# Performance work log

Measured on AMD Instinct MI355X. Metric: run time of the kernel, lower is better.

## Reference

```python
import jax, jax.numpy as jnp
import numpy as np

NUM_HEADS = 32
NUM_KV_HEADS = 8
HEAD_DIM = 128
ROPE_BASE = 10000.0
EPS = 1e-6


def rotate_half(x):
    x1, x2 = jnp.split(x, 2, axis=-1)
    return jnp.concatenate((-x2, x1), axis=-1)


def rms_norm(x, w):
    var = jnp.mean(x * x, axis=-1, keepdims=True)
    return w * (x * jax.lax.rsqrt(var + EPS))


def setup_inputs() -> dict:
    key = jax.random.key(0)
    ks = jax.random.split(key, 5)
    B, S, H = 2, 2048, 4096
    hidden_states = jax.random.normal(ks[0], (B, S, H), dtype=jnp.float32)
    position_ids = jnp.broadcast_to(jnp.arange(S, dtype=jnp.int64), (B, S))
    sc = 1.0 / np.sqrt(H)
    Wq = jax.random.normal(ks[1], (NUM_HEADS * HEAD_DIM, H), dtype=jnp.float32) * sc
    Wk = jax.random.normal(ks[2], (NUM_KV_HEADS * HEAD_DIM, H), dtype=jnp.float32) * sc
    Wv = jax.random.normal(ks[3], (NUM_KV_HEADS * HEAD_DIM, H), dtype=jnp.float32) * sc
    Wo = jax.random.normal(ks[4], (H, NUM_HEADS * HEAD_DIM), dtype=jnp.float32) * sc
    q_norm_w = jnp.ones((HEAD_DIM,), dtype=jnp.float32)
    k_norm_w = jnp.ones((HEAD_DIM,), dtype=jnp.float32)
    return {"hidden_states": hidden_states, "position_ids": position_ids,
            "Wq": Wq, "Wk": Wk, "Wv": Wv, "Wo": Wo,
            "q_norm_w": q_norm_w, "k_norm_w": k_norm_w}


def reference(hidden_states, position_ids, Wq, Wk, Wv, Wo, q_norm_w, k_norm_w):
    B, S, H = hidden_states.shape
    nh, nkv, hd = NUM_HEADS, NUM_KV_HEADS, HEAD_DIM
    groups = nh // nkv

    # QKV projections (Linear, no bias: y = x @ W.T)
    q = (hidden_states @ Wq.T).reshape(B, S, nh, hd)
    k = (hidden_states @ Wk.T).reshape(B, S, nkv, hd)
    v = (hidden_states @ Wv.T).reshape(B, S, nkv, hd)

    # QK RMSNorm over head_dim
    q = rms_norm(q, q_norm_w)
    k = rms_norm(k, k_norm_w)

    # RoPE: cos/sin per position, shape [B, S, hd]
    inv_freq = 1.0 / (ROPE_BASE ** (jnp.arange(0, hd, 2, dtype=jnp.float32) / hd))
    freqs = position_ids.astype(jnp.float32)[..., None] * inv_freq  # [B,S,hd/2]
    emb = jnp.concatenate((freqs, freqs), axis=-1)
    cos = jnp.cos(emb)[:, :, None, :]  # [B,S,1,hd]
    sin = jnp.sin(emb)[:, :, None, :]
    q = q * cos + rotate_half(q) * sin
    k = k * cos + rotate_half(k) * sin

    # GQA: repeat KV heads (repeat_interleave along head axis)
    k = jnp.repeat(k, groups, axis=2)  # [B,S,nh,hd]
    v = jnp.repeat(v, groups, axis=2)

    # Causal SDPA
    scale = 1.0 / np.sqrt(hd)
    scores = jnp.einsum('bqhd,bkhd->bhqk', q, k) * scale
    causal = jnp.tril(jnp.ones((S, S), dtype=bool))
    scores = jnp.where(causal, scores, jnp.finfo(scores.dtype).min)
    probs = jax.nn.softmax(scores, axis=-1)
    attn = jnp.einsum('bhqk,bkhd->bqhd', probs, v).reshape(B, S, nh * hd)

    return attn @ Wo.T
```

## Files before the change

kernel.cpp:

```cpp
#include <hip/hip_runtime.h>

typedef __bf16 bf16;
typedef __bf16 bf16x8 __attribute__((ext_vector_type(8)));
typedef __bf16 bf16x4 __attribute__((ext_vector_type(4)));
typedef float  f32x4  __attribute__((ext_vector_type(4)));

__device__ __forceinline__ void async_copy16(const bf16* g, bf16* l) {
    __builtin_amdgcn_global_load_lds(
        (const __attribute__((address_space(1))) unsigned int*)g,
        (__attribute__((address_space(3))) unsigned int*)l, 16, 0, 0);
}

__global__ __launch_bounds__(256) void cast_bf16(const float* __restrict__ src,
                                                 bf16* __restrict__ dst,
                                                 long long n) {
    long long i = ((long long)blockIdx.x * 256 + threadIdx.x) * 8;
    if (i >= n) return;
    float4 v0 = *(const float4*)&src[i];
    float4 v1 = *(const float4*)&src[i + 4];
    union { int4 v; bf16 h[8]; } u;
    u.h[0] = (bf16)v0.x; u.h[1] = (bf16)v0.y; u.h[2] = (bf16)v0.z; u.h[3] = (bf16)v0.w;
    u.h[4] = (bf16)v1.x; u.h[5] = (bf16)v1.y; u.h[6] = (bf16)v1.z; u.h[7] = (bf16)v1.w;
    *(int4*)&dst[i] = u.v;
}

template <typename OutT>
__global__ __launch_bounds__(256) void gemm_bt(const bf16* __restrict__ A,
                                               const bf16* __restrict__ B,
                                               OutT* __restrict__ C,
                                               int M, int N, int K) {
    __shared__ __attribute__((aligned(16))) bf16 lA[128 * 32];
    __shared__ __attribute__((aligned(16))) bf16 lB[128 * 32];
    const int tid = threadIdx.x, lane = tid & 63, w = tid >> 6;
    const int l16 = lane & 15, quad = lane >> 4;
    const int m0 = blockIdx.y * 128, n0 = blockIdx.x * 128;
    const int wm = (w >> 1) * 64, wn = (w & 1) * 64;

    const int sr = lane >> 2;
    const int sc = (lane & 3) * 8;

    f32x4 acc[4][4];
    for (int mi = 0; mi < 4; ++mi)
        for (int ni = 0; ni < 4; ++ni)
            acc[mi][ni] = f32x4{0.f, 0.f, 0.f, 0.f};

    for (int kb = 0; kb < K; kb += 32) {
        for (int i = 0; i < 2; ++i) {
            int c = i * 4 + w;
            async_copy16(&A[(size_t)(m0 + c * 16 + sr) * K + kb + sc],
                         &lA[c * 512 + lane * 8]);
        }
        for (int i = 0; i < 2; ++i) {
            int c = i * 4 + w;
            async_copy16(&B[(size_t)(n0 + c * 16 + sr) * K + kb + sc],
                         &lB[c * 512 + lane * 8]);
        }
        __syncthreads();
        bf16x8 af[4], bfr[4];
        for (int mi = 0; mi < 4; ++mi)
            af[mi] = *(const bf16x8*)&lA[(wm + mi * 16 + l16) * 32 + quad * 8];
        for (int ni = 0; ni < 4; ++ni)
            bfr[ni] = *(const bf16x8*)&lB[(wn + ni * 16 + l16) * 32 + quad * 8];
        for (int mi = 0; mi < 4; ++mi)
            for (int ni = 0; ni < 4; ++ni)
                acc[mi][ni] = __builtin_amdgcn_mfma_f32_16x16x32_bf16(
                    af[mi], bfr[ni], acc[mi][ni], 0, 0, 0);
        __syncthreads();
    }
    for (int mi = 0; mi < 4; ++mi)
        for (int ni = 0; ni < 4; ++ni) {
            int col = n0 + wn + ni * 16 + l16;
            for (int r = 0; r < 4; ++r) {
                int row = m0 + wm + mi * 16 + quad * 4 + r;
                C[(size_t)row * N + col] = (OutT)acc[mi][ni][r];
            }
        }
}

__global__ __launch_bounds__(256) void rmsnorm_rope(const bf16* __restrict__ qkv,
                                                    const float* __restrict__ qw,
                                                    const float* __restrict__ kw,
                                                    bf16* __restrict__ qb,
                                                    bf16* __restrict__ kb) {
    const int lane = threadIdx.x & 63, w = threadIdx.x >> 6;
    const int j = blockIdx.y * 4 + w;
    const int t = blockIdx.x;
    const int b = t >> 11, s = t & 2047;
    const bool isq = (j < 32);
    const bf16* src = qkv + (size_t)t * 6144 + (isq ? j * 128 : 4096 + (j - 32) * 128);
    float a  = (float)src[lane];
    float bb = (float)src[lane + 64];
    float ss = a * a + bb * bb;
    for (int off = 1; off < 64; off <<= 1) ss += __shfl_xor(ss, off, 64);
    float rms = rsqrtf(ss * (1.f / 128.f) + 1e-6f);
    const float* wn = isq ? qw : kw;
    float an = a * rms * wn[lane];
    float bn = bb * rms * wn[lane + 64];
    float inv_freq = exp2f(-(float)lane * (13.287712379549449f / 64.f));
    float fr = (float)s * inv_freq;
    float c = cosf(fr), sn = sinf(fr);
    float o0 = an * c - bn * sn;
    float o1 = bn * c + an * sn;
    if (isq) {
        const float sc = 0.08838834764831845f * 1.4426950408889634f;
        o0 *= sc; o1 *= sc;
    }
    bf16* dst = isq ? (qb + (((size_t)(b * 32 + j)) * 2048 + s) * 128)
                    : (kb + (((size_t)(b * 8 + (j - 32))) * 2048 + s) * 128);
    dst[lane]      = (bf16)o0;
    dst[lane + 64] = (bf16)o1;
}

__global__ __launch_bounds__(256) void v_transpose(const bf16* __restrict__ qkv,
                                                   bf16* __restrict__ vb) {
    __shared__ __attribute__((aligned(16))) bf16 tile[64][130];
    const int tid = threadIdx.x;
    const int tt = blockIdx.x, kvh = blockIdx.y, b = blockIdx.z;
    const bf16* src = qkv + ((size_t)(b * 2048 + tt * 64)) * 6144 + 5120 + kvh * 128;
    for (int i = 0; i < 4; ++i) {
        int idx = tid + i * 256;
        int r = idx >> 4, c8 = (idx & 15) * 8;
        union { int4 v; bf16 h[8]; } u;
        u.v = *(const int4*)&src[(size_t)r * 6144 + c8];
        for (int jj = 0; jj < 8; ++jj) tile[r][c8 + jj] = u.h[jj];
    }
    __syncthreads();
    bf16* dst = vb + ((size_t)(b * 8 + kvh) * 128) * 2048 + tt * 64;
    for (int i = 0; i < 4; ++i) {
        int idx = tid + i * 256;
        int d = idx >> 3, r8 = (idx & 7) * 8;
        union { int4 v; bf16 h[8]; } u;
        for (int jj = 0; jj < 8; ++jj) u.h[jj] = tile[r8 + jj][d];
        *(int4*)&dst[(size_t)d * 2048 + r8] = u.v;
    }
}

__global__ __launch_bounds__(256, 2) void flash_kernel(const bf16* __restrict__ qb,
                                                       const bf16* __restrict__ kb,
                                                       const bf16* __restrict__ vb,
                                                       bf16* __restrict__ attnb) {
    const int S = 2048;
    const int hp = blockIdx.x;
    const int qt = 31 - blockIdx.y;
    const int b  = blockIdx.z;
    const int h0 = hp * 2, kvh = h0 >> 2;
    const int tid = threadIdx.x, lane = tid & 63, w = tid >> 6;
    const int l16 = lane & 15, quad = lane >> 4;

    __shared__ __attribute__((aligned(16))) bf16 lK[64 * 128];
    __shared__ __attribute__((aligned(16))) bf16 lVt[128 * 64];

    const bf16* Qg0 = qb + (((size_t)(b * 32 + h0)) * S + qt * 64 + w * 16 + l16) * 128;
    const bf16* Qg1 = Qg0 + (size_t)S * 128;
    bf16x8 qf0[4], qf1[4];
    for (int c = 0; c < 4; ++c) {
        qf0[c] = *(const bf16x8*)&Qg0[c * 32 + quad * 8];
        qf1[c] = *(const bf16x8*)&Qg1[c * 32 + quad * 8];
    }

    const bf16* Kg = kb + ((size_t)(b * 8 + kvh)) * S * 128;
    const bf16* Vg = vb + ((size_t)(b * 8 + kvh)) * 128 * S;

    int kOff[4], vOff[4];
    bf16 *kDst[4], *vDst[4];
    for (int i = 0; i < 4; ++i) {
        int c = w * 4 + i;
        int rho = c * 4 + (lane >> 4);
        int prow = (rho & 32) | ((rho & 12) << 1) | ((rho & 16) >> 2) | (rho & 3);
        kOff[i] = prow * 128 + (lane & 15) * 8;
        kDst[i] = lK + c * 512 + lane * 8;
        int d = c * 8 + (lane >> 3);
        vOff[i] = d * S + (lane & 7) * 8;
        vDst[i] = lVt + c * 512 + lane * 8;
    }

    float m0_i = -INFINITY, l0_i = 0.f, m1_i = -INFINITY, l1_i = 0.f;
    f32x4 O0[8], O1[8];
    for (int ti = 0; ti < 8; ++ti) { O0[ti] = f32x4{0.f,0.f,0.f,0.f}; O1[ti] = f32x4{0.f,0.f,0.f,0.f}; }

    for (int kt = 0; kt <= qt; ++kt) {
        const bf16* Kt = Kg + (size_t)kt * 64 * 128;
        const bf16* Vt = Vg + kt * 64;
        for (int i = 0; i < 4; ++i) async_copy16(Kt + kOff[i], kDst[i]);
        for (int i = 0; i < 4; ++i) async_copy16(Vt + vOff[i], vDst[i]);
        __syncthreads();

        f32x4 sT0[4], sT1[4];
        for (int mi = 0; mi < 4; ++mi) { sT0[mi] = f32x4{0.f,0.f,0.f,0.f}; sT1[mi] = f32x4{0.f,0.f,0.f,0.f}; }
        for (int mi = 0; mi < 4; ++mi)
            for (int c = 0; c < 4; ++c) {
                bf16x8 kf = *(const bf16x8*)&lK[(mi * 16 + l16) * 128 + c * 32 + quad * 8];
                sT0[mi] = __builtin_amdgcn_mfma_f32_16x16x32_bf16(kf, qf0[c], sT0[mi], 0, 0, 0);
                sT1[mi] = __builtin_amdgcn_mfma_f32_16x16x32_bf16(kf, qf1[c], sT1[mi], 0, 0, 0);
            }

        if (kt == qt) {
            int qloc = w * 16 + l16;
            for (int mi = 0; mi < 4; ++mi) {
                int kvbase = (mi >> 1) * 32 + quad * 8 + (mi & 1) * 4;
                for (int r = 0; r < 4; ++r)
                    if (kvbase + r > qloc) { sT0[mi][r] = -INFINITY; sT1[mi][r] = -INFINITY; }
            }
        }

        float mx0 = sT0[0][0], mx1 = sT1[0][0];
        for (int mi = 0; mi < 4; ++mi)
            for (int r = 0; r < 4; ++r) { mx0 = fmaxf(mx0, sT0[mi][r]); mx1 = fmaxf(mx1, sT1[mi][r]); }
        mx0 = fmaxf(mx0, __shfl_xor(mx0, 16, 64));
        mx0 = fmaxf(mx0, __shfl_xor(mx0, 32, 64));
        mx1 = fmaxf(mx1, __shfl_xor(mx1, 16, 64));
        mx1 = fmaxf(mx1, __shfl_xor(mx1, 32, 64));
        float mn0 = fmaxf(m0_i, mx0), mn1 = fmaxf(m1_i, mx1);
        float al0 = exp2f(m0_i - mn0), al1 = exp2f(m1_i - mn1);
        m0_i = mn0; m1_i = mn1;

        bf16x8 pbt0[2], pbt1[2];
        float s0 = 0.f, s1 = 0.f;
        for (int mi = 0; mi < 4; ++mi) {
            int t = mi >> 1, o = (mi & 1) * 4;
            for (int r = 0; r < 4; ++r) {
                float p0 = exp2f(sT0[mi][r] - mn0);
                float p1 = exp2f(sT1[mi][r] - mn1);
                s0 += p0; s1 += p1;
                pbt0[t][o + r] = (bf16)p0;
                pbt1[t][o + r] = (bf16)p1;
            }
        }
        s0 += __shfl_xor(s0, 16, 64); s0 += __shfl_xor(s0, 32, 64);
        s1 += __shfl_xor(s1, 16, 64); s1 += __shfl_xor(s1, 32, 64);
        l0_i = l0_i * al0 + s0;
        l1_i = l1_i * al1 + s1;
        for (int ti = 0; ti < 8; ++ti) { O0[ti] *= al0; O1[ti] *= al1; }

        for (int ti = 0; ti < 8; ++ti)
            for (int t = 0; t < 2; ++t) {
                bf16x8 vf = *(const bf16x8*)&lVt[(ti * 16 + l16) * 64 + t * 32 + quad * 8];
                O0[ti] = __builtin_amdgcn_mfma_f32_16x16x32_bf16(vf, pbt0[t], O0[ti], 0, 0, 0);
                O1[ti] = __builtin_amdgcn_mfma_f32_16x16x32_bf16(vf, pbt1[t], O1[ti], 0, 0, 0);
            }
        __syncthreads();
    }

    float i0 = 1.f / l0_i, i1 = 1.f / l1_i;
    bf16* dst = attnb + (((size_t)(b * S + qt * 64 + w * 16 + l16)) * 4096) + h0 * 128 + quad * 4;
    for (int ti = 0; ti < 8; ++ti) {
        bf16x4 o4, o5;
        for (int r = 0; r < 4; ++r) { o4[r] = (bf16)(O0[ti][r] * i0); o5[r] = (bf16)(O1[ti][r] * i1); }
        *(bf16x4*)&dst[ti * 16] = o4;
        *(bf16x4*)&dst[128 + ti * 16] = o5;
    }
}

extern "C" void kernel_launch(void* const* d_in, const int* in_sizes, int n_in,
                              void* d_out, int out_size, void* d_ws, size_t ws_size,
                              hipStream_t stream) {
    const float* X  = (const float*)d_in[0];
    const float* Wq = (const float*)d_in[2];
    const float* Wk = (const float*)d_in[3];
    const float* Wv = (const float*)d_in[4];
    const float* Wo = (const float*)d_in[5];
    const float* qw = (const float*)d_in[6];
    const float* kw = (const float*)d_in[7];
    float* out = (float*)d_out;
    char* ws = (char*)d_ws;

    bf16* Xb    = (bf16*)(ws);
    bf16* Wqkvb = (bf16*)(ws + 33554432);
    bf16* QKVb  = (bf16*)(ws + 83886080);
    bf16* qbuf  = (bf16*)(ws);
    bf16* kbuf  = (bf16*)(ws + 33554432);
    bf16* vbuf  = (bf16*)(ws + 41943040);
    bf16* Wob   = (bf16*)(ws + 50331648);
    bf16* attnb = (bf16*)(ws + 83886080);

    cast_bf16<<<8192, 256, 0, stream>>>(X, Xb, 16777216);
    cast_bf16<<<8192, 256, 0, stream>>>(Wq, Wqkvb, 16777216);
    cast_bf16<<<2048, 256, 0, stream>>>(Wk, Wqkvb + 16777216, 4194304);
    cast_bf16<<<2048, 256, 0, stream>>>(Wv, Wqkvb + 20971520, 4194304);

    gemm_bt<bf16><<<dim3(48, 32), 256, 0, stream>>>(Xb, Wqkvb, QKVb, 4096, 6144, 4096);

    rmsnorm_rope<<<dim3(4096, 10), 256, 0, stream>>>(QKVb, qw, kw, qbuf, kbuf);
    v_transpose<<<dim3(32, 8, 2), 256, 0, stream>>>(QKVb, vbuf);
    cast_bf16<<<8192, 256, 0, stream>>>(Wo, Wob, 16777216);

    flash_kernel<<<dim3(16, 32, 2), 256, 0, stream>>>(qbuf, kbuf, vbuf, attnb);

    gemm_bt<float><<<dim3(32, 32), 256, 0, stream>>>(attnb, Wob, out, 4096, 4096, 4096);
}
```

Before: 871.7 us.

## Replace GEMM with 256x256 tiled, multi-stage pipelined, LDS-swizzled MFMA kernel

Replaces the simple 128x128 single-buffered GEMM with a 512-thread kernel computing 256x256 tiles, using a 4-slot ring of async global-to-LDS copies that prefetch three K-tiles ahead. Reads and writes to LDS use an XOR swizzle to reduce bank conflicts, and MFMA phases run at raised wave priority, separated by barriers. The larger tiles increase data reuse per load, and the pipelining hides memory latency. In exchange, the kernel uses 128KB of LDS and many accumulator registers, and the grid has fewer blocks, which may leave CUs unevenly loaded.

```diff
diff --git a/kernel.cpp b/kernel.cpp
--- a/kernel.cpp
+++ b/kernel.cpp
@@ -25,53 +25,118 @@
 }
 
 template <typename OutT>
-__global__ __launch_bounds__(256) void gemm_bt(const bf16* __restrict__ A,
-                                               const bf16* __restrict__ B,
-                                               OutT* __restrict__ C,
-                                               int M, int N, int K) {
-    __shared__ __attribute__((aligned(16))) bf16 lA[128 * 32];
-    __shared__ __attribute__((aligned(16))) bf16 lB[128 * 32];
+__global__ __launch_bounds__(512, 2) void gemm256(const bf16* __restrict__ A,
+                                                  const bf16* __restrict__ B,
+                                                  OutT* __restrict__ C,
+                                                  int M, int N, int K) {
+    __shared__ __attribute__((aligned(16))) bf16 sm[65536];
+
     const int tid = threadIdx.x, lane = tid & 63, w = tid >> 6;
     const int l16 = lane & 15, quad = lane >> 4;
-    const int m0 = blockIdx.y * 128, n0 = blockIdx.x * 128;
-    const int wm = (w >> 1) * 64, wn = (w & 1) * 64;
-
-    const int sr = lane >> 2;
-    const int sc = (lane & 3) * 8;
-
-    f32x4 acc[4][4];
-    for (int mi = 0; mi < 4; ++mi)
+    const int wr = w >> 2, wc = w & 3;
+    const int m0 = blockIdx.y * 256, n0 = blockIdx.x * 256;
+
+    const int srow = lane >> 2;
+    const int scol = 8 * ((lane & 3) ^ ((lane >> 3) & 3));
+    const bf16* gA0 = A + (size_t)(m0 + w * 16 + srow) * K + scol;
+    const bf16* gA1 = A + (size_t)(m0 + (8 + w) * 16 + srow) * K + scol;
+    const bf16* gB0 = B + (size_t)(n0 + w * 16 + srow) * K + scol;
+    const bf16* gB1 = B + (size_t)(n0 + (8 + w) * 16 + srow) * K + scol;
+
+    const int rcol = 8 * (quad ^ ((l16 >> 1) & 3));
+
+    f32x4 acc[8][4];
+#pragma unroll
+    for (int mi = 0; mi < 8; ++mi)
+#pragma unroll
         for (int ni = 0; ni < 4; ++ni)
             acc[mi][ni] = f32x4{0.f, 0.f, 0.f, 0.f};
 
-    for (int kb = 0; kb < K; kb += 32) {
-        for (int i = 0; i < 2; ++i) {
-            int c = i * 4 + w;
-            async_copy16(&A[(size_t)(m0 + c * 16 + sr) * K + kb + sc],
-                         &lA[c * 512 + lane * 8]);
-        }
-        for (int i = 0; i < 2; ++i) {
-            int c = i * 4 + w;
-            async_copy16(&B[(size_t)(n0 + c * 16 + sr) * K + kb + sc],
-                         &lB[c * 512 + lane * 8]);
-        }
-        __syncthreads();
-        bf16x8 af[4], bfr[4];
-        for (int mi = 0; mi < 4; ++mi)
-            af[mi] = *(const bf16x8*)&lA[(wm + mi * 16 + l16) * 32 + quad * 8];
-        for (int ni = 0; ni < 4; ++ni)
-            bfr[ni] = *(const bf16x8*)&lB[(wn + ni * 16 + l16) * 32 + quad * 8];
-        for (int mi = 0; mi < 4; ++mi)
-            for (int ni = 0; ni < 4; ++ni)
-                acc[mi][ni] = __builtin_amdgcn_mfma_f32_16x16x32_bf16(
-                    af[mi], bfr[ni], acc[mi][ni], 0, 0, 0);
-        __syncthreads();
-    }
-    for (int mi = 0; mi < 4; ++mi)
+    const int NT = K >> 5;
+
+    for (int pt = 0; pt < 3; ++pt) {
+        bf16* sa = &sm[pt * 8192];
+        bf16* sb = &sm[32768 + pt * 8192];
+        const int ko = pt * 32;
+        async_copy16(gA0 + ko, sa + w * 512 + lane * 8);
+        async_copy16(gB0 + ko, sb + w * 512 + lane * 8);
+        async_copy16(gA1 + ko, sa + (8 + w) * 512 + lane * 8);
+        async_copy16(gB1 + ko, sb + (8 + w) * 512 + lane * 8);
+    }
+    asm volatile("s_waitcnt vmcnt(8)" ::: "memory");
+    __builtin_amdgcn_s_barrier();
+    __builtin_amdgcn_sched_barrier(0);
+
+#define GTILE(T, DO_STAGE, VMN)                                                   \
+    {                                                                             \
+        const int q_ = (T) & 3;                                                   \
+        const bf16* a_ = &sm[q_ * 8192];                                          \
+        const bf16* b_ = &sm[32768 + q_ * 8192];                                  \
+        bf16x8 af[8], bf0, bf1;                                                   \
+        _Pragma("unroll")                                                         \
+        for (int mi = 0; mi < 8; ++mi)                                            \
+            af[mi] = *(const bf16x8*)&a_[(wr * 128 + mi * 16 + l16) * 32 + rcol]; \
+        bf0 = *(const bf16x8*)&b_[(wc * 64 + l16) * 32 + rcol];                   \
+        bf1 = *(const bf16x8*)&b_[(wc * 64 + 16 + l16) * 32 + rcol];              \
+        if (DO_STAGE) {                                                           \
+            const int ko_ = ((T) + 3) * 32;                                       \
+            bf16* sa_ = &sm[(((T) + 3) & 3) * 8192];                              \
+            bf16* sb_ = &sm[32768 + (((T) + 3) & 3) * 8192];                      \
+            async_copy16(gA0 + ko_, sa_ + w * 512 + lane * 8);                    \
+            async_copy16(gB0 + ko_, sb_ + w * 512 + lane * 8);                    \
+        }                                                                         \
+        __builtin_amdgcn_s_barrier();                                             \
+        __builtin_amdgcn_sched_barrier(0);                                        \
+        __builtin_amdgcn_s_setprio(1);                                            \
+        _Pragma("unroll")                                                         \
+        for (int mi = 0; mi < 8; ++mi) {                                          \
+            acc[mi][0] = __builtin_amdgcn_mfma_f32_16x16x32_bf16(af[mi], bf0,     \
+                                                       acc[mi][0], 0, 0, 0);      \
+            acc[mi][1] = __builtin_amdgcn_mfma_f32_16x16x32_bf16(af[mi], bf1,     \
+                                                       acc[mi][1], 0, 0, 0);      \
+        }                                                                         \
+        __builtin_amdgcn_s_setprio(0);                                            \
+        __builtin_amdgcn_s_barrier();                                             \
+        __builtin_amdgcn_sched_barrier(0);                                        \
+        bf0 = *(const bf16x8*)&b_[(wc * 64 + 32 + l16) * 32 + rcol];              \
+        bf1 = *(const bf16x8*)&b_[(wc * 64 + 48 + l16) * 32 + rcol];              \
+        if (DO_STAGE) {                                                           \
+            const int ko_ = ((T) + 3) * 32;                                       \
+            bf16* sa_ = &sm[(((T) + 3) & 3) * 8192];                              \
+            bf16* sb_ = &sm[32768 + (((T) + 3) & 3) * 8192];                      \
+            async_copy16(gA1 + ko_, sa_ + (8 + w) * 512 + lane * 8);              \
+            async_copy16(gB1 + ko_, sb_ + (8 + w) * 512 + lane * 8);              \
+        }                                                                         \
+        __builtin_amdgcn_s_barrier();                                             \
+        __builtin_amdgcn_sched_barrier(0);                                        \
+        __builtin_amdgcn_s_setprio(1);                                            \
+        _Pragma("unroll")                                                         \
+        for (int mi = 0; mi < 8; ++mi) {                                          \
+            acc[mi][2] = __builtin_amdgcn_mfma_f32_16x16x32_bf16(af[mi], bf0,     \
+                                                       acc[mi][2], 0, 0, 0);      \
+            acc[mi][3] = __builtin_amdgcn_mfma_f32_16x16x32_bf16(af[mi], bf1,     \
+                                                       acc[mi][3], 0, 0, 0);      \
+        }                                                                         \
+        __builtin_amdgcn_s_setprio(0);                                            \
+        asm volatile("s_waitcnt vmcnt(" #VMN ")" ::: "memory");                   \
+        __builtin_amdgcn_s_barrier();                                             \
+        __builtin_amdgcn_sched_barrier(0);                                        \
+    }
+
+    for (int t = 0; t < NT - 3; ++t) GTILE(t, 1, 8)
+    GTILE(NT - 3, 0, 4)
+    GTILE(NT - 2, 0, 0)
+    GTILE(NT - 1, 0, 0)
+#undef GTILE
+
+#pragma unroll
+    for (int mi = 0; mi < 8; ++mi)
+#pragma unroll
         for (int ni = 0; ni < 4; ++ni) {
-            int col = n0 + wn + ni * 16 + l16;
+            int col = n0 + wc * 64 + ni * 16 + l16;
+#pragma unroll
             for (int r = 0; r < 4; ++r) {
-                int row = m0 + wm + mi * 16 + quad * 4 + r;
+                int row = m0 + wr * 128 + mi * 16 + quad * 4 + r;
                 C[(size_t)row * N + col] = (OutT)acc[mi][ni][r];
             }
         }
@@ -278,7 +343,7 @@
     cast_bf16<<<2048, 256, 0, stream>>>(Wk, Wqkvb + 16777216, 4194304);
     cast_bf16<<<2048, 256, 0, stream>>>(Wv, Wqkvb + 20971520, 4194304);
 
-    gemm_bt<bf16><<<dim3(48, 32), 256, 0, stream>>>(Xb, Wqkvb, QKVb, 4096, 6144, 4096);
+    gemm256<bf16><<<dim3(24, 16), 512, 0, stream>>>(Xb, Wqkvb, QKVb, 4096, 6144, 4096);
 
     rmsnorm_rope<<<dim3(4096, 10), 256, 0, stream>>>(QKVb, qw, kw, qbuf, kbuf);
     v_transpose<<<dim3(32, 8, 2), 256, 0, stream>>>(QKVb, vbuf);
@@ -286,5 +351,5 @@
 
     flash_kernel<<<dim3(16, 32, 2), 256, 0, stream>>>(qbuf, kbuf, vbuf, attnb);
 
-    gemm_bt<float><<<dim3(32, 32), 256, 0, stream>>>(attnb, Wob, out, 4096, 4096, 4096);
-}
+    gemm256<float><<<dim3(16, 16), 512, 0, stream>>>(attnb, Wob, out, 4096, 4096, 4096);
+}
```

After: 750.5 us. 13.9% less time.

## Replace GEMM with 256x256 tile, 8-wave pipelined kernel with swizzled LDS

Applied to the files above, without the earlier changes.

Replaces the simple 128x128 single-buffered GEMM with a 256x256-tile, 512-thread kernel using double-buffered LDS, BK=64, and XOR-swizzled LDS layout. Async global-to-LDS loads for the next stages are interleaved with MFMA phases, with barriers and setprio to overlap memory and compute. This is meant to cut the sync stalls and LDS bank conflicts of the old kernel and raise arithmetic intensity per block. In exchange it uses 128KB of LDS per block and many accumulator registers, and the grid for the QKV and output GEMMs shrinks to 384 and 256 blocks, which may underfill the CUs.

```diff
diff --git a/kernel.cpp b/kernel.cpp
--- a/kernel.cpp
+++ b/kernel.cpp
@@ -25,53 +25,172 @@
 }
 
 template <typename OutT>
-__global__ __launch_bounds__(256) void gemm_bt(const bf16* __restrict__ A,
-                                               const bf16* __restrict__ B,
-                                               OutT* __restrict__ C,
-                                               int M, int N, int K) {
-    __shared__ __attribute__((aligned(16))) bf16 lA[128 * 32];
-    __shared__ __attribute__((aligned(16))) bf16 lB[128 * 32];
+__global__ __launch_bounds__(512, 2) void gemm8p(const bf16* __restrict__ A,
+                                                 const bf16* __restrict__ B,
+                                                 OutT* __restrict__ C,
+                                                 int M, int N, int K) {
+    __shared__ __attribute__((aligned(16))) bf16 sm[65536];
+
     const int tid = threadIdx.x, lane = tid & 63, w = tid >> 6;
     const int l16 = lane & 15, quad = lane >> 4;
-    const int m0 = blockIdx.y * 128, n0 = blockIdx.x * 128;
-    const int wm = (w >> 1) * 64, wn = (w & 1) * 64;
-
-    const int sr = lane >> 2;
-    const int sc = (lane & 3) * 8;
-
-    f32x4 acc[4][4];
-    for (int mi = 0; mi < 4; ++mi)
+    const int wr = w >> 2, wc = w & 3;
+    const int m0 = blockIdx.y * 256, n0 = blockIdx.x * 256;
+
+    const int srow = lane >> 3;
+    const int scol = 8 * ((lane & 7) ^ srow);
+    const int rsw  = l16 & 7;
+
+    f32x4 acc[8][4];
+#pragma unroll
+    for (int mi = 0; mi < 8; ++mi)
+#pragma unroll
         for (int ni = 0; ni < 4; ++ni)
             acc[mi][ni] = f32x4{0.f, 0.f, 0.f, 0.f};
 
-    for (int kb = 0; kb < K; kb += 32) {
+    const int NT = K >> 6;
+
+    auto stgA = [&](int h, bf16* la, int ko) {
+        const int r0 = h * 64 + w * 8;
+        async_copy16(A + (size_t)(m0 + r0 + srow) * K + ko + scol,
+                     la + r0 * 64 + lane * 8);
+        const int r1 = 128 + h * 64 + w * 8;
+        async_copy16(A + (size_t)(m0 + r1 + srow) * K + ko + scol,
+                     la + r1 * 64 + lane * 8);
+    };
+    auto stgB = [&](int nh, bf16* lb, int ko) {
+#pragma unroll
         for (int i = 0; i < 2; ++i) {
-            int c = i * 4 + w;
-            async_copy16(&A[(size_t)(m0 + c * 16 + sr) * K + kb + sc],
-                         &lA[c * 512 + lane * 8]);
+            int idx = i * 8 + w;
+            int r = (idx >> 2) * 64 + nh * 32 + (idx & 3) * 8;
+            async_copy16(B + (size_t)(n0 + r + srow) * K + ko + scol,
+                         lb + r * 64 + lane * 8);
         }
-        for (int i = 0; i < 2; ++i) {
-            int c = i * 4 + w;
-            async_copy16(&B[(size_t)(n0 + c * 16 + sr) * K + kb + sc],
-                         &lB[c * 512 + lane * 8]);
+    };
+
+#define RDA(h)                                                                  \
+    _Pragma("unroll") for (int i2 = 0; i2 < 4; ++i2)                            \
+        _Pragma("unroll") for (int kk = 0; kk < 2; ++kk)                        \
+            af[i2][kk] = *(const bf16x8*)&a_[(wr * 128 + ((h) * 4 + i2) * 16 +  \
+                                              l16) * 64 +                       \
+                                             8 * (((kk << 2) | quad) ^ rsw)];
+#define RDB(nh)                                                                 \
+    _Pragma("unroll") for (int j2 = 0; j2 < 2; ++j2)                            \
+        _Pragma("unroll") for (int kk = 0; kk < 2; ++kk)                        \
+            bfr[j2][kk] = *(const bf16x8*)&b_[(wc * 64 + ((nh) * 2 + j2) * 16 + \
+                                               l16) * 64 +                      \
+                                              8 * (((kk << 2) | quad) ^ rsw)];
+#define MM(h, nh)                                                               \
+    _Pragma("unroll") for (int i2 = 0; i2 < 4; ++i2)                            \
+        _Pragma("unroll") for (int j2 = 0; j2 < 2; ++j2) {                      \
+            acc[(h) * 4 + i2][(nh) * 2 + j2] =                                  \
+                __builtin_amdgcn_mfma_f32_16x16x32_bf16(                        \
+                    af[i2][0], bfr[j2][0], acc[(h) * 4 + i2][(nh) * 2 + j2],    \
+                    0, 0, 0);                                                   \
+            acc[(h) * 4 + i2][(nh) * 2 + j2] =                                  \
+                __builtin_amdgcn_mfma_f32_16x16x32_bf16(                        \
+                    af[i2][1], bfr[j2][1], acc[(h) * 4 + i2][(nh) * 2 + j2],    \
+                    0, 0, 0);                                                   \
         }
-        __syncthreads();
-        bf16x8 af[4], bfr[4];
-        for (int mi = 0; mi < 4; ++mi)
-            af[mi] = *(const bf16x8*)&lA[(wm + mi * 16 + l16) * 32 + quad * 8];
-        for (int ni = 0; ni < 4; ++ni)
-            bfr[ni] = *(const bf16x8*)&lB[(wn + ni * 16 + l16) * 32 + quad * 8];
-        for (int mi = 0; mi < 4; ++mi)
-            for (int ni = 0; ni < 4; ++ni)
-                acc[mi][ni] = __builtin_amdgcn_mfma_f32_16x16x32_bf16(
-                    af[mi], bfr[ni], acc[mi][ni], 0, 0, 0);
-        __syncthreads();
-    }
-    for (int mi = 0; mi < 4; ++mi)
+#define FENCE_MFMA                                                              \
+    __builtin_amdgcn_sched_barrier(0);                                          \
+    __builtin_amdgcn_s_barrier();                                               \
+    asm volatile("s_waitcnt lgkmcnt(0)" ::: "memory");                          \
+    __builtin_amdgcn_sched_barrier(0);                                          \
+    __builtin_amdgcn_s_setprio(1);
+#define ENDPH                                                                   \
+    __builtin_amdgcn_s_setprio(0);                                              \
+    __builtin_amdgcn_sched_barrier(0);                                          \
+    __builtin_amdgcn_s_barrier();                                               \
+    __builtin_amdgcn_sched_barrier(0);
+
+    stgB(0, sm + 16384, 0); stgA(0, sm, 0); stgB(1, sm + 16384, 0); stgA(1, sm, 0);
+    stgA(0, sm + 32768, 64); stgB(1, sm + 49152, 64); stgA(1, sm + 32768, 64);
+    asm volatile("s_waitcnt vmcnt(6)" ::: "memory");
+    __builtin_amdgcn_s_barrier();
+    __builtin_amdgcn_sched_barrier(0);
+
+    for (int s = 0; s < NT - 2; ++s) {
+        const int p = s & 1;
+        bf16* a_ = sm + p * 32768;
+        bf16* b_ = sm + 16384 + p * 32768;
+        bf16* aS = a_;
+        bf16* bS = b_;
+        bf16* bO = sm + 16384 + (1 - p) * 32768;
+        const int ko1 = (s + 1) << 6, ko2 = (s + 2) << 6;
+        bf16x8 af[4][2], bfr[2][2];
+
+        RDA(0) RDB(0) stgB(0, bO, ko1);
+        FENCE_MFMA; MM(0, 0) ENDPH;
+
+        RDB(1) stgA(0, aS, ko2);
+        FENCE_MFMA; MM(0, 1) ENDPH;
+
+        RDA(1) stgB(1, bS, ko2);
+        FENCE_MFMA; MM(1, 1) ENDPH;
+
+        RDB(0) stgA(1, aS, ko2);
+        FENCE_MFMA; MM(1, 0)
+        __builtin_amdgcn_s_setprio(0);
+        __builtin_amdgcn_sched_barrier(0);
+        asm volatile("s_waitcnt vmcnt(6)" ::: "memory");
+        __builtin_amdgcn_s_barrier();
+        __builtin_amdgcn_sched_barrier(0);
+    }
+
+    {
+        const int p = (NT - 2) & 1;
+        bf16* a_ = sm + p * 32768;
+        bf16* b_ = sm + 16384 + p * 32768;
+        bf16* bO = sm + 16384 + (1 - p) * 32768;
+        const int ko1 = (NT - 1) << 6;
+        bf16x8 af[4][2], bfr[2][2];
+
+        RDA(0) RDB(0) stgB(0, bO, ko1);
+        FENCE_MFMA; MM(0, 0) ENDPH;
+        RDB(1)
+        FENCE_MFMA; MM(0, 1) ENDPH;
+        RDA(1)
+        FENCE_MFMA; MM(1, 1) ENDPH;
+        RDB(0)
+        FENCE_MFMA; MM(1, 0)
+        __builtin_amdgcn_s_setprio(0);
+        __builtin_amdgcn_sched_barrier(0);
+        asm volatile("s_waitcnt vmcnt(0)" ::: "memory");
+        __builtin_amdgcn_s_barrier();
+        __builtin_amdgcn_sched_barrier(0);
+    }
+
+    {
+        const int p = (NT - 1) & 1;
+        bf16* a_ = sm + p * 32768;
+        bf16* b_ = sm + 16384 + p * 32768;
+        bf16x8 af[4][2], bfr[2][2];
+
+        RDA(0) RDB(0)
+        FENCE_MFMA; MM(0, 0) ENDPH;
+        RDB(1)
+        FENCE_MFMA; MM(0, 1) ENDPH;
+        RDA(1)
+        FENCE_MFMA; MM(1, 1) ENDPH;
+        RDB(0)
+        FENCE_MFMA; MM(1, 0)
+        __builtin_amdgcn_s_setprio(0);
+        __builtin_amdgcn_sched_barrier(0);
+    }
+#undef RDA
+#undef RDB
+#undef MM
+#undef FENCE_MFMA
+#undef ENDPH
+
+#pragma unroll
+    for (int mi = 0; mi < 8; ++mi)
+#pragma unroll
         for (int ni = 0; ni < 4; ++ni) {
-            int col = n0 + wn + ni * 16 + l16;
+            int col = n0 + wc * 64 + ni * 16 + l16;
+#pragma unroll
             for (int r = 0; r < 4; ++r) {
-                int row = m0 + wm + mi * 16 + quad * 4 + r;
+                int row = m0 + wr * 128 + mi * 16 + quad * 4 + r;
                 C[(size_t)row * N + col] = (OutT)acc[mi][ni][r];
             }
         }
@@ -278,7 +397,7 @@
     cast_bf16<<<2048, 256, 0, stream>>>(Wk, Wqkvb + 16777216, 4194304);
     cast_bf16<<<2048, 256, 0, stream>>>(Wv, Wqkvb + 20971520, 4194304);
 
-    gemm_bt<bf16><<<dim3(48, 32), 256, 0, stream>>>(Xb, Wqkvb, QKVb, 4096, 6144, 4096);
+    gemm8p<bf16><<<dim3(24, 16), 512, 0, stream>>>(Xb, Wqkvb, QKVb, 4096, 6144, 4096);
 
     rmsnorm_rope<<<dim3(4096, 10), 256, 0, stream>>>(QKVb, qw, kw, qbuf, kbuf);
     v_transpose<<<dim3(32, 8, 2), 256, 0, stream>>>(QKVb, vbuf);
@@ -286,5 +405,5 @@
 
     flash_kernel<<<dim3(16, 32, 2), 256, 0, stream>>>(qbuf, kbuf, vbuf, attnb);
 
-    gemm_bt<float><<<dim3(32, 32), 256, 0, stream>>>(attnb, Wob, out, 4096, 4096, 4096);
-}
+    gemm8p<float><<<dim3(16, 16), 512, 0, stream>>>(attnb, Wob, out, 4096, 4096, 4096);
+}
```

Result: faster. 731.6 us (-16.1%).
